# Kernel tuning notes

Hardware: AMD Instinct MI355X
Metric: run time of the kernel (lower is better)

Reference implementation:

```python
import jax, jax.numpy as jnp
import numpy as np

D_MODEL = 768
D_STATE = 128
D_CONV = 4
EXPAND = 2
HEADDIM = 64
NGROUPS = 1
D_INNER = EXPAND * D_MODEL            # 1536
NHEADS = D_INNER // HEADDIM           # 24
CONV_DIM = D_INNER + 2 * NGROUPS * D_STATE  # 1792
D_IN_PROJ = 2 * D_INNER + 2 * NGROUPS * D_STATE + NHEADS  # 3352
EPS = 1e-5


def setup_inputs() -> dict:
    key = jax.random.key(0)
    ks = jax.random.split(key, 8)
    b, l = 4, 2048
    return {
        "feature": jax.random.normal(ks[0], (b, l, D_MODEL), jnp.float32),
        "in_proj_w": jax.random.normal(ks[1], (D_IN_PROJ, D_MODEL), jnp.float32) * 0.02,
        "conv_w": jax.random.normal(ks[2], (CONV_DIM, D_CONV), jnp.float32) * 0.2,
        "conv_b": jnp.zeros((CONV_DIM,), jnp.float32),
        "dt_bias": jax.random.normal(ks[3], (NHEADS,), jnp.float32) * 0.1,
        # A in [1,16) -> A_log = log(A)
        "A_log": jnp.log(1.0 + 15.0 * jax.random.uniform(ks[4], (NHEADS,), jnp.float32)),
        "D": jnp.ones((NHEADS,), jnp.float32),
        "norm_w": jnp.ones((D_INNER,), jnp.float32),
        "out_proj_w": jax.random.normal(ks[5], (D_MODEL, D_INNER), jnp.float32) * 0.02,
        "gate1": jnp.float32(0.6),
    }


def _mamba2(u, in_proj_w, conv_w, conv_b, dt_bias, A_log, D, norm_w, out_proj_w):
    b, l, _ = u.shape
    zxbcdt = jnp.einsum('bld,ed->ble', u, in_proj_w)  # [b,l,3352]
    z, xBC, dt = jnp.split(zxbcdt, [D_INNER, D_INNER + CONV_DIM], axis=-1)
    dt = jax.nn.softplus(dt + dt_bias)  # [b,l,h]

    # causal depthwise conv1d + silu on xBC
    xc = jnp.transpose(xBC, (0, 2, 1))  # [b,c,l]
    xc = jax.lax.conv_general_dilated(
        xc, conv_w[:, None, :], (1,), [(D_CONV - 1, 0)],
        dimension_numbers=('NCH', 'OIH', 'NCH'), feature_group_count=CONV_DIM)
    xBC = jax.nn.silu(jnp.transpose(xc, (0, 2, 1)) + conv_b)

    x, B, C = jnp.split(xBC, [D_INNER, D_INNER + NGROUPS * D_STATE], axis=-1)
    x = x.reshape(b, l, NHEADS, HEADDIM)
    A = -jnp.exp(A_log)          # [h], negative
    dA = jnp.exp(dt * A)         # [b,l,h]

    def step(h, inp):
        # h: [b,h,p,n]
        dA_t, dt_t, x_t, B_t, C_t = inp  # [b,h],[b,h],[b,h,p],[b,n],[b,n]
        h = h * dA_t[..., None, None] + (dt_t[..., None] * x_t)[..., None] * B_t[:, None, None, :]
        y = jnp.einsum('bhpn,bn->bhp', h, C_t)
        return h, y

    h0 = jnp.zeros((b, NHEADS, HEADDIM, D_STATE), u.dtype)
    xs = (jnp.moveaxis(dA, 1, 0), jnp.moveaxis(dt, 1, 0), jnp.moveaxis(x, 1, 0),
          jnp.moveaxis(B, 1, 0), jnp.moveaxis(C, 1, 0))
    _, ys = jax.lax.scan(step, h0, xs)           # [l,b,h,p]
    y = jnp.moveaxis(ys, 0, 1) + x * D[None, None, :, None]
    y = y.reshape(b, l, D_INNER)

    # gated RMSNorm: gate then normalize (norm_before_gate=False)
    y = y * jax.nn.silu(z)
    y = y * jax.lax.rsqrt(jnp.mean(y * y, axis=-1, keepdims=True) + EPS) * norm_w
    return jnp.einsum('bld,ed->ble', y, out_proj_w)


def reference(feature, in_proj_w, conv_w, conv_b, dt_bias, A_log, D, norm_w, out_proj_w, gate1):
    out = _mamba2(feature, in_proj_w, conv_w, conv_b, dt_bias, A_log, D, norm_w, out_proj_w)
    return jax.nn.sigmoid(gate1) * out
```

## Files before the change

kernel.cpp:

```cpp
#include <hip/hip_runtime.h>
#include <cstddef>

#define NB 4
#define SEQL 2048
#define DMODEL 768
#define DSTATE 128
#define HEADDIM 64
#define NHEADS 24
#define DINNER 1536
#define CONVDIM 1792
#define DINPROJ 3352
#define BLROWS (NB*SEQL)
#define RMS_EPS 1e-5f
#define Q 128
#define NC (SEQL/Q)
#define BOFF DINNER
#define COFF (DINNER + DSTATE)
#define BK 64

typedef unsigned int uint;
typedef unsigned short ushort;
typedef __attribute__((ext_vector_type(8))) short bf16x8;
typedef __attribute__((ext_vector_type(4))) float f32x4;

__device__ __forceinline__ float sigmoidf_(float x){ return 1.f/(1.f+expf(-x)); }
__device__ __forceinline__ float siluf_(float x){ return x * sigmoidf_(x); }
__device__ __forceinline__ float softplusf_(float x){ return x > 20.f ? x : log1pf(expf(x)); }

__device__ __forceinline__ ushort f2bf(float f){
    union { float f; uint u; } v; v.f = f;
    uint r = (v.u + 0x7FFFu + ((v.u >> 16) & 1u)) >> 16;
    return (ushort)r;
}
__device__ __forceinline__ float bf2f(ushort s){
    union { uint u; float f; } v; v.u = ((uint)s) << 16;
    return v.f;
}
__device__ __forceinline__ uint pack2(float a, float b){
    return (uint)f2bf(a) | ((uint)f2bf(b) << 16);
}
__device__ __forceinline__ void unpack8(uint4 r, float* o){
    o[0]=bf2f((ushort)(r.x&0xffff)); o[1]=bf2f((ushort)(r.x>>16));
    o[2]=bf2f((ushort)(r.y&0xffff)); o[3]=bf2f((ushort)(r.y>>16));
    o[4]=bf2f((ushort)(r.z&0xffff)); o[5]=bf2f((ushort)(r.z>>16));
    o[6]=bf2f((ushort)(r.w&0xffff)); o[7]=bf2f((ushort)(r.w>>16));
}
__device__ __forceinline__ uint packu2(ushort a, ushort b){
    return (uint)a | ((uint)b << 16);
}

#define GLD16(g, l) __builtin_amdgcn_global_load_lds( \
    (const __attribute__((address_space(1))) void*)(g), \
    (__attribute__((address_space(3))) void*)(l), 16, 0, 0)

__global__ __launch_bounds__(256) void cast_kernel(
    const float* __restrict__ in, ushort* __restrict__ out, int n4)
{
    const int i = blockIdx.x*256 + threadIdx.x;
    if (i < n4) {
        float4 v = ((const float4*)in)[i];
        ushort4 o = make_ushort4(f2bf(v.x), f2bf(v.y), f2bf(v.z), f2bf(v.w));
        ((ushort4*)out)[i] = o;
    }
}

__global__ __launch_bounds__(256) void gemm_mfma(
    const ushort* __restrict__ A, const ushort* __restrict__ W,
    float* __restrict__ C, int M, int N, int K, int nxblk,
    const float* __restrict__ gptr)
{
    __shared__ __align__(16) ushort sm[2*128*BK*2];
    const int tid = threadIdx.x;
    const int wv = tid >> 6, ln = tid & 63;
    const int id = blockIdx.x;
    const int xcd = id & 7;
    const int local = id >> 3;
    const int m0 = (xcd*8 + (local & 7)) * 128;
    const int n0 = (local >> 3) * 128;
    const int wm = (wv >> 1) * 64, wn = (wv & 1) * 64;

    const int sr = ln >> 3;
    const int scol = ((ln & 7) ^ sr) * 8;
    const ushort* gA[4]; const ushort* gB[4];
    ushort* lA[4]; ushort* lB[4];
#pragma unroll
    for (int iss = 0; iss < 4; ++iss) {
        const int ra = m0 + wv*32 + iss*8 + sr;
        gA[iss] = A + (size_t)ra * K + scol;
        int rb = n0 + wv*32 + iss*8 + sr; if (rb >= N) rb = N - 1;
        gB[iss] = W + (size_t)rb * K + scol;
        lA[iss] = &sm[(wv*32 + iss*8) * BK];
        lB[iss] = &sm[8192 + (wv*32 + iss*8) * BK];
    }

    f32x4 acc[4][4];
#pragma unroll
    for (int i = 0; i < 4; ++i)
#pragma unroll
        for (int j = 0; j < 4; ++j) acc[i][j] = (f32x4){0.f, 0.f, 0.f, 0.f};

    const int fr = ln & 15;
    const int fq = ln >> 4;
    const int nt = K / BK;

#pragma unroll
    for (int iss = 0; iss < 4; ++iss) {
        GLD16(gA[iss], lA[iss]);
        GLD16(gB[iss], lB[iss]);
    }

    for (int kt = 0; kt < nt; ++kt) {
        if (kt + 1 < nt) {
            const int so = ((kt + 1) & 1) * 16384;
            const int ko = (kt + 1) * BK;
#pragma unroll
            for (int iss = 0; iss < 4; ++iss) {
                GLD16(gA[iss] + ko, lA[iss] + so);
                GLD16(gB[iss] + ko, lB[iss] + so);
            }
            asm volatile("s_waitcnt vmcnt(8)" ::: "memory");
        } else {
            asm volatile("s_waitcnt vmcnt(0)" ::: "memory");
        }
        __builtin_amdgcn_s_barrier();
        const ushort* As = sm + (kt & 1) * 16384;
        const ushort* Bs = As + 8192;
#pragma unroll
        for (int kh = 0; kh < 2; ++kh) {
            const int sw = ((kh*4 + fq) ^ (fr & 7)) * 8;
            bf16x8 af[4], bfr[4];
#pragma unroll
            for (int i = 0; i < 4; ++i)
                af[i] = *(const bf16x8*)&As[(wm + i*16 + fr)*BK + sw];
#pragma unroll
            for (int j = 0; j < 4; ++j)
                bfr[j] = *(const bf16x8*)&Bs[(wn + j*16 + fr)*BK + sw];
#pragma unroll
            for (int i = 0; i < 4; ++i)
#pragma unroll
                for (int j = 0; j < 4; ++j)
                    acc[i][j] = __builtin_amdgcn_mfma_f32_16x16x32_bf16(af[i], bfr[j], acc[i][j], 0, 0, 0);
        }
        __builtin_amdgcn_s_barrier();
    }

    float scale = 1.f;
    if (gptr) scale = sigmoidf_(*gptr);
    const int cn = ln & 15;
    const int cr = (ln >> 4) * 4;
#pragma unroll
    for (int i = 0; i < 4; ++i) {
        const int mb = m0 + wm + i*16 + cr;
#pragma unroll
        for (int j = 0; j < 4; ++j) {
            const int n = n0 + wn + j*16 + cn;
            if (n < N) {
                float* cp = C + (size_t)mb * N + n;
                cp[0*(size_t)N] = acc[i][j].x * scale;
                cp[1*(size_t)N] = acc[i][j].y * scale;
                cp[2*(size_t)N] = acc[i][j].z * scale;
                cp[3*(size_t)N] = acc[i][j].w * scale;
            }
        }
    }
}

__global__ __launch_bounds__(256) void gemm_mfma_bf16o(
    const ushort* __restrict__ A, const ushort* __restrict__ W,
    ushort* __restrict__ C, float* __restrict__ dtraw, int M, int N, int K)
{
    __shared__ __align__(16) ushort sm[2*128*BK*2];
    const int tid = threadIdx.x;
    const int wv = tid >> 6, ln = tid & 63;
    const int id = blockIdx.x;
    const int xcd = id & 7;
    const int local = id >> 3;
    const int m0 = (xcd*8 + (local & 7)) * 128;
    const int n0 = (local >> 3) * 128;
    const int wm = (wv >> 1) * 64, wn = (wv & 1) * 64;

    const int sr = ln >> 3;
    const int scol = ((ln & 7) ^ sr) * 8;
    const ushort* gA[4]; const ushort* gB[4];
    ushort* lA[4]; ushort* lB[4];
#pragma unroll
    for (int iss = 0; iss < 4; ++iss) {
        const int ra = m0 + wv*32 + iss*8 + sr;
        gA[iss] = A + (size_t)ra * K + scol;
        int rb = n0 + wv*32 + iss*8 + sr; if (rb >= N) rb = N - 1;
        gB[iss] = W + (size_t)rb * K + scol;
        lA[iss] = &sm[(wv*32 + iss*8) * BK];
        lB[iss] = &sm[8192 + (wv*32 + iss*8) * BK];
    }

    f32x4 acc[4][4];
#pragma unroll
    for (int i = 0; i < 4; ++i)
#pragma unroll
        for (int j = 0; j < 4; ++j) acc[i][j] = (f32x4){0.f, 0.f, 0.f, 0.f};

    const int fr = ln & 15;
    const int fq = ln >> 4;
    const int nt = K / BK;

#pragma unroll
    for (int iss = 0; iss < 4; ++iss) {
        GLD16(gA[iss], lA[iss]);
        GLD16(gB[iss], lB[iss]);
    }

    for (int kt = 0; kt < nt; ++kt) {
        if (kt + 1 < nt) {
            const int so = ((kt + 1) & 1) * 16384;
            const int ko = (kt + 1) * BK;
#pragma unroll
            for (int iss = 0; iss < 4; ++iss) {
                GLD16(gA[iss] + ko, lA[iss] + so);
                GLD16(gB[iss] + ko, lB[iss] + so);
            }
            asm volatile("s_waitcnt vmcnt(8)" ::: "memory");
        } else {
            asm volatile("s_waitcnt vmcnt(0)" ::: "memory");
        }
        __builtin_amdgcn_s_barrier();
        const ushort* As = sm + (kt & 1) * 16384;
        const ushort* Bs = As + 8192;
#pragma unroll
        for (int kh = 0; kh < 2; ++kh) {
            const int sw = ((kh*4 + fq) ^ (fr & 7)) * 8;
            bf16x8 af[4], bfr[4];
#pragma unroll
            for (int i = 0; i < 4; ++i)
                af[i] = *(const bf16x8*)&As[(wm + i*16 + fr)*BK + sw];
#pragma unroll
            for (int j = 0; j < 4; ++j)
                bfr[j] = *(const bf16x8*)&Bs[(wn + j*16 + fr)*BK + sw];
#pragma unroll
            for (int i = 0; i < 4; ++i)
#pragma unroll
                for (int j = 0; j < 4; ++j)
                    acc[i][j] = __builtin_amdgcn_mfma_f32_16x16x32_bf16(af[i], bfr[j], acc[i][j], 0, 0, 0);
        }
        __builtin_amdgcn_s_barrier();
    }

    const int cn = ln & 15;
    const int cr = (ln >> 4) * 4;
    __syncthreads();
    ushort* rp = sm + wv*4096;
#pragma unroll
    for (int i = 0; i < 4; ++i)
#pragma unroll
        for (int j = 0; j < 4; ++j) {
            const int col = j*16 + cn;
#pragma unroll
            for (int r = 0; r < 4; ++r)
                rp[(i*16 + cr + r)*64 + col] = f2bf(acc[i][j][r]);
        }
    __syncthreads();
#pragma unroll
    for (int k2 = 0; k2 < 8; ++k2) {
        const int row = k2*8 + (ln >> 3);
        uint4 v = *(const uint4*)&rp[row*64 + (ln & 7)*8];
        const int gm = m0 + wm + row;
        const int gn = n0 + wn + (ln & 7)*8;
        if (gn + 8 <= N)
            *(uint4*)(C + (size_t)gm*N + gn) = v;
    }
    if (n0 + 128 > N) {
#pragma unroll
        for (int i = 0; i < 4; ++i) {
            const int mb = m0 + wm + i*16 + cr;
#pragma unroll
            for (int j = 0; j < 4; ++j) {
                const int col = (n0 + wn + j*16 + cn) - (N - 24);
                if (col >= 0 && col < 24) {
                    dtraw[(size_t)(mb+0)*24 + col] = acc[i][j].x;
                    dtraw[(size_t)(mb+1)*24 + col] = acc[i][j].y;
                    dtraw[(size_t)(mb+2)*24 + col] = acc[i][j].z;
                    dtraw[(size_t)(mb+3)*24 + col] = acc[i][j].w;
                }
            }
        }
    }
}

__global__ __launch_bounds__(448) void conv_kernel(
    const ushort* __restrict__ zx, const float* __restrict__ conv_w,
    const float* __restrict__ conv_b, ushort* __restrict__ xconv)
{
    const int c4 = threadIdx.x;
    const int bl = blockIdx.x;
    const int l = bl & (SEQL - 1);
    float w[4][4];
#pragma unroll
    for (int j = 0; j < 4; ++j) {
        float4 wr = *(const float4*)(conv_w + (c4*4 + j)*4);
        w[j][0]=wr.x; w[j][1]=wr.y; w[j][2]=wr.z; w[j][3]=wr.w;
    }
    float4 bias = *(const float4*)(conv_b + c4*4);
    float s[4] = {bias.x, bias.y, bias.z, bias.w};
#pragma unroll
    for (int k = 0; k < 4; ++k) {
        const int ls = l - 3 + k;
        if (ls >= 0) {
            ushort4 xv = *(const ushort4*)(zx + (size_t)(bl - 3 + k)*DINPROJ + DINNER + c4*4);
            s[0] = fmaf(bf2f(xv.x), w[0][k], s[0]);
            s[1] = fmaf(bf2f(xv.y), w[1][k], s[1]);
            s[2] = fmaf(bf2f(xv.z), w[2][k], s[2]);
            s[3] = fmaf(bf2f(xv.w), w[3][k], s[3]);
        }
    }
    ushort4 o = make_ushort4(f2bf(siluf_(s[0])), f2bf(siluf_(s[1])),
                             f2bf(siluf_(s[2])), f2bf(siluf_(s[3])));
    *(ushort4*)(xconv + (size_t)bl*CONVDIM + c4*4) = o;
}

__global__ __launch_bounds__(128) void dtscan_kernel(
    const float* __restrict__ dtraw, const float* __restrict__ dt_bias,
    const float* __restrict__ A_log, float* __restrict__ dtc, float* __restrict__ clog)
{
    const int c = blockIdx.x, h = blockIdx.y, b = blockIdx.z;
    const int t = threadIdx.x;
    const int bl = b*SEQL + c*Q + t;
    float draw = dtraw[(size_t)bl*24 + h] + dt_bias[h];
    float dtv = softplusf_(draw);
    float la = -expf(A_log[h]) * dtv;
    const int lane = t & 63;
    float v = la;
#pragma unroll
    for (int off = 1; off < 64; off <<= 1) {
        float u = __shfl_up(v, off);
        if (lane >= off) v += u;
    }
    __shared__ float w0tot;
    if (t == 63) w0tot = v;
    __syncthreads();
    if (t >= 64) v += w0tot;
    const int idx = (b*NHEADS + h)*SEQL + c*Q + t;
    dtc[idx] = dtv;
    clog[idx] = v;
}

__global__ __launch_bounds__(256) void gcb_mfma(
    const ushort* __restrict__ xconv, ushort* __restrict__ G)
{
    __shared__ __align__(16) ushort Ca[64*32];
    __shared__ __align__(16) ushort Bb[128*32];
    const int thalf = blockIdx.x, c = blockIdx.y, b = blockIdx.z;
    const int tid = threadIdx.x;
    const int wv = tid >> 6, ln = tid & 63;
    const int fr = ln & 15, fq = ln >> 4, fk = fq*8;
    const int bl0 = b*SEQL + c*Q;
    const int th0 = thalf*64;

    const int sat = tid & 63,  sac = (tid >> 6)*8;
    const int sbt = tid & 127, sbh = (tid >> 7)*16;

    f32x4 acc[4][2];
#pragma unroll
    for (int i = 0; i < 4; ++i)
#pragma unroll
        for (int j = 0; j < 2; ++j) acc[i][j] = (f32x4){0.f,0.f,0.f,0.f};

    for (int ks = 0; ks < 4; ++ks) {
        uint4 av = *(const uint4*)(xconv + (size_t)(bl0 + th0 + sat)*CONVDIM + COFF + ks*32 + sac);
        const ushort* br = xconv + (size_t)(bl0 + sbt)*CONVDIM + BOFF + ks*32 + sbh;
        uint4 bv0 = *(const uint4*)br;
        uint4 bv1 = *(const uint4*)(br + 8);
        __syncthreads();
        *(uint4*)&Ca[sat*32 + sac] = av;
        *(uint4*)&Bb[sbt*32 + sbh] = bv0;
        *(uint4*)&Bb[sbt*32 + sbh + 8] = bv1;
        __syncthreads();
        bf16x8 av_[4], bv_[2];
#pragma unroll
        for (int i = 0; i < 4; ++i)
            av_[i] = *(const bf16x8*)&Ca[(i*16 + fr)*32 + fk];
#pragma unroll
        for (int j = 0; j < 2; ++j)
            bv_[j] = *(const bf16x8*)&Bb[(wv*32 + j*16 + fr)*32 + fk];
#pragma unroll
        for (int i = 0; i < 4; ++i)
#pragma unroll
            for (int j = 0; j < 2; ++j)
                acc[i][j] = __builtin_amdgcn_mfma_f32_16x16x32_bf16(av_[i], bv_[j], acc[i][j], 0, 0, 0);
    }
    ushort* gout = G + (size_t)(b*NC + c)*(Q*Q);
#pragma unroll
    for (int i = 0; i < 4; ++i) {
#pragma unroll
        for (int j = 0; j < 2; ++j) {
            const int s = wv*32 + j*16 + fr;
#pragma unroll
            for (int r = 0; r < 4; ++r) {
                const int t = th0 + i*16 + fq*4 + r;
                gout[t*Q + s] = f2bf(acc[i][j][r]);
            }
        }
    }
}

#define ASTR 40
#define BSTR 40
__global__ __launch_bounds__(256) void locstate_mfma(
    const ushort* __restrict__ xconv, const float* __restrict__ dtc,
    const float* __restrict__ clog, ushort* __restrict__ Sloc)
{
    __shared__ __align__(16) ushort Ab[64*ASTR];
    __shared__ __align__(16) ushort Bb[128*BSTR];
    __shared__ float sw[Q];
    const int c = blockIdx.x, h = blockIdx.y, b = blockIdx.z;
    const int tid = threadIdx.x;
    const int wv = tid >> 6, ln = tid & 63;
    const int fr = ln & 15, fq = ln >> 4, fk = fq*8;
    const int bh = b*NHEADS + h;
    const int bl0 = b*SEQL + c*Q;

    if (tid < Q) {
        const float ce = clog[(size_t)bh*SEQL + c*Q + (Q-1)];
        const float cs = clog[(size_t)bh*SEQL + c*Q + tid];
        sw[tid] = dtc[(size_t)bh*SEQL + c*Q + tid] * expf(ce - cs);
    }
    __syncthreads();

    f32x4 acc[4][2];
#pragma unroll
    for (int i = 0; i < 4; ++i)
#pragma unroll
        for (int j = 0; j < 2; ++j) acc[i][j] = (f32x4){0.f,0.f,0.f,0.f};

    const int ap = tid & 63, aoct = tid >> 6;
    const int bn = tid & 127, bhalf = tid >> 7;

    for (int ks = 0; ks < 4; ++ks) {
        float xv[8];
#pragma unroll
        for (int j = 0; j < 8; ++j) {
            const int s = ks*32 + aoct*8 + j;
            xv[j] = bf2f(xconv[(size_t)(bl0 + s)*CONVDIM + h*HEADDIM + ap]) * sw[s];
        }
        ushort bu[16];
#pragma unroll
        for (int j = 0; j < 16; ++j) {
            const int s = ks*32 + bhalf*16 + j;
            bu[j] = xconv[(size_t)(bl0 + s)*CONVDIM + BOFF + bn];
        }
        __syncthreads();
        *(uint4*)&Ab[ap*ASTR + aoct*8] =
            make_uint4(pack2(xv[0],xv[1]), pack2(xv[2],xv[3]),
                       pack2(xv[4],xv[5]), pack2(xv[6],xv[7]));
        *(uint4*)&Bb[bn*BSTR + bhalf*16] =
            make_uint4(packu2(bu[0],bu[1]), packu2(bu[2],bu[3]),
                       packu2(bu[4],bu[5]), packu2(bu[6],bu[7]));
        *(uint4*)&Bb[bn*BSTR + bhalf*16 + 8] =
            make_uint4(packu2(bu[8],bu[9]), packu2(bu[10],bu[11]),
                       packu2(bu[12],bu[13]), packu2(bu[14],bu[15]));
        __syncthreads();
        bf16x8 af[4], bf[2];
#pragma unroll
        for (int i = 0; i < 4; ++i)
            af[i] = *(const bf16x8*)&Ab[(i*16 + fr)*ASTR + fk];
#pragma unroll
        for (int j = 0; j < 2; ++j)
            bf[j] = *(const bf16x8*)&Bb[(wv*32 + j*16 + fr)*BSTR + fk];
#pragma unroll
        for (int i = 0; i < 4; ++i)
#pragma unroll
            for (int j = 0; j < 2; ++j)
                acc[i][j] = __builtin_amdgcn_mfma_f32_16x16x32_bf16(af[i], bf[j], acc[i][j], 0, 0, 0);
    }
    ushort* dst = Sloc + (size_t)((b*NC + c)*NHEADS + h) * (HEADDIM*DSTATE);
#pragma unroll
    for (int i = 0; i < 4; ++i) {
#pragma unroll
        for (int j = 0; j < 2; ++j) {
            const int n = wv*32 + j*16 + fr;
#pragma unroll
            for (int r = 0; r < 4; ++r) {
                const int p = i*16 + fq*4 + r;
                dst[p*DSTATE + n] = f2bf(acc[i][j][r]);
            }
        }
    }
}

__global__ __launch_bounds__(256) void chunkscan_kernel(
    const float* __restrict__ clog, ushort* __restrict__ S)
{
    const int h = blockIdx.x, b = blockIdx.y, pg = blockIdx.z;
    const int tid = threadIdx.x;
    const int p = pg*16 + (tid >> 4);
    const int n0 = (tid & 15) * 8;
    const int bh = b*NHEADS + h;
    float st[8];
#pragma unroll
    for (int j = 0; j < 8; ++j) st[j] = 0.f;

    for (int c = 0; c < NC; ++c) {
        const float tc = expf(clog[(size_t)bh*SEQL + c*Q + (Q-1)]);
        ushort* base = S + (size_t)((b*NC + c)*NHEADS + h) * (HEADDIM*DSTATE);
        uint4 raw = *(uint4*)(base + p*DSTATE + n0);
        float lv[8];
        unpack8(raw, lv);
        uint4 pre = make_uint4(pack2(st[0],st[1]), pack2(st[2],st[3]),
                               pack2(st[4],st[5]), pack2(st[6],st[7]));
        *(uint4*)(base + p*DSTATE + n0) = pre;
#pragma unroll
        for (int j = 0; j < 8; ++j) st[j] = fmaf(tc, st[j], lv[j]);
    }
}

__global__ __launch_bounds__(256) void ychunk_mfma(
    const ushort* __restrict__ xconv, const float* __restrict__ dtc,
    const float* __restrict__ clog, const ushort* __restrict__ G,
    const ushort* __restrict__ Sp, const float* __restrict__ Dv,
    ushort* __restrict__ ybf)
{
    __shared__ __align__(16) ushort smu[8192];
    ushort* Ab = smu;
    ushort* Bb = smu + 4096;
    __shared__ float s_clog[Q];
    __shared__ float s_dtc[Q];
    const int c = blockIdx.x, h = blockIdx.y, b = blockIdx.z;
    const int tid = threadIdx.x;
    const int wv = tid >> 6, ln = tid & 63;
    const int bh = b*NHEADS + h;
    const int bl0 = b*SEQL + c*Q;
    const int fr = ln & 15, fq = ln >> 4, fk = fq*8;

    if (tid < Q) {
        s_clog[tid] = clog[(size_t)bh*SEQL + c*Q + tid];
        s_dtc[tid]  = dtc [(size_t)bh*SEQL + c*Q + tid];
    }

    f32x4 acc[2][4];
#pragma unroll
    for (int i = 0; i < 2; ++i)
#pragma unroll
        for (int j = 0; j < 4; ++j) acc[i][j] = (f32x4){0.f,0.f,0.f,0.f};

    const int sgt = tid & 127, sgh = (tid >> 7)*16;
    const int sbp = tid & 63,  sbc = (tid >> 6)*8;
    const ushort* spb = Sp + (size_t)((b*NC + c)*NHEADS + h)*(HEADDIM*DSTATE);

    for (int ks = 0; ks < 4; ++ks) {
        const ushort* cr = xconv + (size_t)(bl0 + sgt)*CONVDIM + COFF + ks*32 + sgh;
        uint4 cv0 = *(const uint4*)cr;
        uint4 cv1 = *(const uint4*)(cr + 8);
        uint4 sv = *(const uint4*)(spb + sbp*DSTATE + ks*32 + sbc);
        __syncthreads();
        *(uint4*)&Ab[sgt*32 + sgh]     = cv0;
        *(uint4*)&Ab[sgt*32 + sgh + 8] = cv1;
        *(uint4*)&Bb[sbp*32 + sbc] = sv;
        __syncthreads();
        bf16x8 af[2], bv[4];
        af[0] = *(const bf16x8*)&Ab[(wv*32 +      fr)*32 + fk];
        af[1] = *(const bf16x8*)&Ab[(wv*32 + 16 + fr)*32 + fk];
#pragma unroll
        for (int j = 0; j < 4; ++j)
            bv[j] = *(const bf16x8*)&Bb[(j*16 + fr)*32 + fk];
#pragma unroll
        for (int i = 0; i < 2; ++i)
#pragma unroll
            for (int j = 0; j < 4; ++j)
                acc[i][j] = __builtin_amdgcn_mfma_f32_16x16x32_bf16(af[i], bv[j], acc[i][j], 0, 0, 0);
    }
#pragma unroll
    for (int i = 0; i < 2; ++i) {
        const int tb = wv*32 + i*16 + fq*4;
        float e0 = expf(s_clog[tb+0]), e1 = expf(s_clog[tb+1]);
        float e2 = expf(s_clog[tb+2]), e3 = expf(s_clog[tb+3]);
#pragma unroll
        for (int j = 0; j < 4; ++j) {
            acc[i][j].x *= e0; acc[i][j].y *= e1; acc[i][j].z *= e2; acc[i][j].w *= e3;
        }
    }

    const ushort* gp = G + (size_t)(b*NC + c)*(Q*Q);
    for (int ks = 0; ks < 4; ++ks) {
        uint4 g0 = *(const uint4*)(gp + sgt*Q + ks*32 + sgh);
        uint4 g1 = *(const uint4*)(gp + sgt*Q + ks*32 + sgh + 8);
        ushort xu[8];
#pragma unroll
        for (int j = 0; j < 8; ++j)
            xu[j] = xconv[(size_t)(bl0 + ks*32 + sbc + j)*CONVDIM + h*HEADDIM + sbp];
        __syncthreads();
        {
            float gvals[16];
            unpack8(g0, gvals);
            unpack8(g1, gvals + 8);
            const float ct = s_clog[sgt];
            ushort gw[16];
#pragma unroll
            for (int j = 0; j < 16; ++j) {
                const int s = ks*32 + sgh + j;
                float w = 0.f;
                if (s <= sgt) w = s_dtc[s] * expf(ct - s_clog[s]);
                gw[j] = f2bf(gvals[j] * w);
            }
            *(uint4*)&Ab[sgt*32 + sgh] =
                make_uint4(packu2(gw[0],gw[1]), packu2(gw[2],gw[3]),
                           packu2(gw[4],gw[5]), packu2(gw[6],gw[7]));
            *(uint4*)&Ab[sgt*32 + sgh + 8] =
                make_uint4(packu2(gw[8],gw[9]), packu2(gw[10],gw[11]),
                           packu2(gw[12],gw[13]), packu2(gw[14],gw[15]));
            *(uint4*)&Bb[sbp*32 + sbc] =
                make_uint4(packu2(xu[0],xu[1]), packu2(xu[2],xu[3]),
                           packu2(xu[4],xu[5]), packu2(xu[6],xu[7]));
        }
        __syncthreads();
        if (ks <= wv) {
            bf16x8 af[2], bv[4];
            af[0] = *(const bf16x8*)&Ab[(wv*32 +      fr)*32 + fk];
            af[1] = *(const bf16x8*)&Ab[(wv*32 + 16 + fr)*32 + fk];
#pragma unroll
            for (int j = 0; j < 4; ++j)
                bv[j] = *(const bf16x8*)&Bb[(j*16 + fr)*32 + fk];
#pragma unroll
            for (int i = 0; i < 2; ++i)
#pragma unroll
                for (int j = 0; j < 4; ++j)
                    acc[i][j] = __builtin_amdgcn_mfma_f32_16x16x32_bf16(af[i], bv[j], acc[i][j], 0, 0, 0);
        }
    }

    const float Dh = Dv[h];
    __syncthreads();
    ushort* rp = smu;
#pragma unroll
    for (int i = 0; i < 2; ++i) {
#pragma unroll
        for (int r = 0; r < 4; ++r) {
            const int t = wv*32 + i*16 + fq*4 + r;
            const ushort* xr = xconv + (size_t)(bl0 + t)*CONVDIM + h*HEADDIM;
#pragma unroll
            for (int j = 0; j < 4; ++j) {
                const int p = j*16 + fr;
                rp[t*64 + p] = f2bf(acc[i][j][r] + Dh * bf2f(xr[p]));
            }
        }
    }
#pragma unroll
    for (int k2 = 0; k2 < 4; ++k2) {
        const int row = wv*32 + k2*8 + (ln >> 3);
        uint4 v = *(const uint4*)&rp[row*64 + (ln & 7)*8];
        *(uint4*)(ybf + (size_t)(bl0 + row)*DINNER + h*HEADDIM + (ln & 7)*8) = v;
    }
}

__global__ __launch_bounds__(128) void rms_kernel(
    const ushort* __restrict__ zx, const float* __restrict__ norm_w,
    ushort* __restrict__ ybf)
{
    const int row = blockIdx.x;
    const int tid = threadIdx.x;
    const ushort* zr = zx + (size_t)row * DINPROJ;
    ushort* yr = ybf + (size_t)row * DINNER;
    float v[12];
    float ss = 0.f;
#pragma unroll
    for (int i = 0; i < 3; ++i) {
        const int o = (tid + i*128) * 4;
        ushort4 yv = *(const ushort4*)(yr + o);
        ushort4 zv = *(const ushort4*)(zr + o);
        float a = bf2f(yv.x) * siluf_(bf2f(zv.x));
        float b = bf2f(yv.y) * siluf_(bf2f(zv.y));
        float cc = bf2f(yv.z) * siluf_(bf2f(zv.z));
        float d = bf2f(yv.w) * siluf_(bf2f(zv.w));
        v[i*4+0]=a; v[i*4+1]=b; v[i*4+2]=cc; v[i*4+3]=d;
        ss += a*a + b*b + cc*cc + d*d;
    }
#pragma unroll
    for (int off = 1; off < 64; off <<= 1) ss += __shfl_xor(ss, off);
    __shared__ float red[2];
    if ((tid & 63) == 0) red[tid >> 6] = ss;
    __syncthreads();
    const float rstd = rsqrtf((red[0] + red[1]) * (1.f/DINNER) + RMS_EPS);
#pragma unroll
    for (int i = 0; i < 3; ++i) {
        const int o = (tid + i*128) * 4;
        float4 wv = *(const float4*)(norm_w + o);
        ushort4 ov = make_ushort4(f2bf(v[i*4+0]*rstd*wv.x), f2bf(v[i*4+1]*rstd*wv.y),
                                  f2bf(v[i*4+2]*rstd*wv.z), f2bf(v[i*4+3]*rstd*wv.w));
        *(ushort4*)(yr + o) = ov;
    }
}

extern "C" void kernel_launch(void* const* d_in, const int* in_sizes, int n_in,
                              void* d_out, int out_size, void* d_ws, size_t ws_size,
                              hipStream_t stream)
{
    const float* feature    = (const float*)d_in[0];
    const float* in_proj_w  = (const float*)d_in[1];
    const float* conv_w     = (const float*)d_in[2];
    const float* conv_b     = (const float*)d_in[3];
    const float* dt_bias    = (const float*)d_in[4];
    const float* A_log      = (const float*)d_in[5];
    const float* Dvec       = (const float*)d_in[6];
    const float* norm_w     = (const float*)d_in[7];
    const float* out_proj_w = (const float*)d_in[8];
    const float* gate1      = (const float*)d_in[9];
    float* out = (float*)d_out;

    ushort* zx    = (ushort*)d_ws;
    ushort* xconv = zx + (size_t)BLROWS * DINPROJ;
    ushort* ybf   = xconv + (size_t)BLROWS * CONVDIM;
    float* dtraw  = (float*)(ybf + (size_t)BLROWS * DINNER);
    float* dtc    = dtraw + (size_t)BLROWS * 24;
    float* clog   = dtc + (size_t)NB * NHEADS * SEQL;
    ushort* Gbuf  = (ushort*)(clog + (size_t)NB * NHEADS * SEQL);
    ushort* Sbuf  = Gbuf + (size_t)NB * NC * Q * Q;
    ushort* Abf    = Gbuf;
    ushort* Wbf_in = Gbuf + (size_t)BLROWS * DMODEL;
    ushort* Wbf_out = zx;

    cast_kernel<<<dim3((BLROWS*DMODEL/4 + 255)/256), 256, 0, stream>>>(feature, Abf, BLROWS*DMODEL/4);
    cast_kernel<<<dim3((DINPROJ*DMODEL/4 + 255)/256), 256, 0, stream>>>(in_proj_w, Wbf_in, DINPROJ*DMODEL/4);
    gemm_mfma_bf16o<<<dim3(27*64), 256, 0, stream>>>(Abf, Wbf_in, zx, dtraw,
                                                     BLROWS, DINPROJ, DMODEL);
    conv_kernel<<<dim3(BLROWS), 448, 0, stream>>>(zx, conv_w, conv_b, xconv);
    dtscan_kernel<<<dim3(NC, NHEADS, NB), 128, 0, stream>>>(dtraw, dt_bias, A_log, dtc, clog);
    gcb_mfma<<<dim3(2, NC, NB), 256, 0, stream>>>(xconv, Gbuf);
    locstate_mfma<<<dim3(NC, NHEADS, NB), 256, 0, stream>>>(xconv, dtc, clog, Sbuf);
    chunkscan_kernel<<<dim3(NHEADS, NB, 4), 256, 0, stream>>>(clog, Sbuf);
    ychunk_mfma<<<dim3(NC, NHEADS, NB), 256, 0, stream>>>(xconv, dtc, clog, Gbuf, Sbuf, Dvec, ybf);
    rms_kernel<<<dim3(BLROWS), 128, 0, stream>>>(zx, norm_w, ybf);
    cast_kernel<<<dim3((DMODEL*DINNER/4 + 255)/256), 256, 0, stream>>>(out_proj_w, Wbf_out, DMODEL*DINNER/4);
    gemm_mfma<<<dim3(6*64), 256, 0, stream>>>(ybf, Wbf_out, out,
                                              BLROWS, DMODEL, DINNER, 6, gate1);
}
```

Baseline: 308.4 us.

## Narrow out-proj GEMM tiles, swizzle epilogue LDS, and sliding-window conv over 16 rows

The output projection GEMM now uses 128x64 tiles, giving 768 blocks instead of 384 so more of the compute units are busy on the N=768 problem. The bf16-output GEMM epilogue XOR-swizzles its LDS staging buffer to avoid bank conflicts on the transposed readback. The conv kernel now has each block process 16 consecutive rows and keep a register sliding window, which cuts the redundant reads of the 3 previous rows. The trade-off is lower per-block data reuse in the out GEMM and fewer conv blocks, each with a longer serial loop.

After: 285.8 us. 1.08x faster.

```diff
diff --git a/kernel.cpp b/kernel.cpp
--- a/kernel.cpp
+++ b/kernel.cpp
@@ -66,8 +66,107 @@
 
 __global__ __launch_bounds__(256) void gemm_mfma(
     const ushort* __restrict__ A, const ushort* __restrict__ W,
-    float* __restrict__ C, int M, int N, int K, int nxblk,
+    float* __restrict__ C, int M, int N, int K,
     const float* __restrict__ gptr)
+{
+    __shared__ __align__(16) ushort sm[2*12288];
+    const int tid = threadIdx.x;
+    const int wv = tid >> 6, ln = tid & 63;
+    const int id = blockIdx.x;
+    const int xcd = id & 7;
+    const int local = id >> 3;
+    const int m0 = (xcd*8 + (local & 7)) * 128;
+    const int n0 = (local >> 3) * 64;
+    const int wm = (wv >> 1) * 64, wn = (wv & 1) * 32;
+
+    const int sr = ln >> 3;
+    const int scol = ((ln & 7) ^ sr) * 8;
+    const ushort* gA[4]; ushort* lA[4];
+#pragma unroll
+    for (int iss = 0; iss < 4; ++iss) {
+        gA[iss] = A + (size_t)(m0 + wv*32 + iss*8 + sr) * K + scol;
+        lA[iss] = &sm[(wv*32 + iss*8) * BK];
+    }
+    const ushort* gB[2]; ushort* lB[2];
+#pragma unroll
+    for (int iss = 0; iss < 2; ++iss) {
+        gB[iss] = W + (size_t)(n0 + wv*16 + iss*8 + sr) * K + scol;
+        lB[iss] = &sm[8192 + (wv*16 + iss*8) * BK];
+    }
+
+    f32x4 acc[4][2];
+#pragma unroll
+    for (int i = 0; i < 4; ++i)
+#pragma unroll
+        for (int j = 0; j < 2; ++j) acc[i][j] = (f32x4){0.f, 0.f, 0.f, 0.f};
+
+    const int fr = ln & 15;
+    const int fq = ln >> 4;
+    const int nt = K / BK;
+
+#pragma unroll
+    for (int iss = 0; iss < 4; ++iss) GLD16(gA[iss], lA[iss]);
+#pragma unroll
+    for (int iss = 0; iss < 2; ++iss) GLD16(gB[iss], lB[iss]);
+
+    for (int kt = 0; kt < nt; ++kt) {
+        if (kt + 1 < nt) {
+            const int so = ((kt + 1) & 1) * 12288;
+            const int ko = (kt + 1) * BK;
+#pragma unroll
+            for (int iss = 0; iss < 4; ++iss) GLD16(gA[iss] + ko, lA[iss] + so);
+#pragma unroll
+            for (int iss = 0; iss < 2; ++iss) GLD16(gB[iss] + ko, lB[iss] + so);
+            asm volatile("s_waitcnt vmcnt(6)" ::: "memory");
+        } else {
+            asm volatile("s_waitcnt vmcnt(0)" ::: "memory");
+        }
+        __builtin_amdgcn_s_barrier();
+        const ushort* As = sm + (kt & 1) * 12288;
+        const ushort* Bs = As + 8192;
+#pragma unroll
+        for (int kh = 0; kh < 2; ++kh) {
+            const int sw = ((kh*4 + fq) ^ (fr & 7)) * 8;
+            bf16x8 af[4], bfr[2];
+#pragma unroll
+            for (int i = 0; i < 4; ++i)
+                af[i] = *(const bf16x8*)&As[(wm + i*16 + fr)*BK + sw];
+#pragma unroll
+            for (int j = 0; j < 2; ++j)
+                bfr[j] = *(const bf16x8*)&Bs[(wn + j*16 + fr)*BK + sw];
+#pragma unroll
+            for (int i = 0; i < 4; ++i)
+#pragma unroll
+                for (int j = 0; j < 2; ++j)
+                    acc[i][j] = __builtin_amdgcn_mfma_f32_16x16x32_bf16(af[i], bfr[j], acc[i][j], 0, 0, 0);
+        }
+        __builtin_amdgcn_s_barrier();
+    }
+
+    float scale = 1.f;
+    if (gptr) scale = sigmoidf_(*gptr);
+    const int cn = ln & 15;
+    const int cr = (ln >> 4) * 4;
+#pragma unroll
+    for (int i = 0; i < 4; ++i) {
+        const int mb = m0 + wm + i*16 + cr;
+#pragma unroll
+        for (int j = 0; j < 2; ++j) {
+            const int n = n0 + wn + j*16 + cn;
+            if (n < N) {
+                float* cp = C + (size_t)mb * N + n;
+                cp[0*(size_t)N] = acc[i][j].x * scale;
+                cp[1*(size_t)N] = acc[i][j].y * scale;
+                cp[2*(size_t)N] = acc[i][j].z * scale;
+                cp[3*(size_t)N] = acc[i][j].w * scale;
+            }
+        }
+    }
+}
+
+__global__ __launch_bounds__(256) void gemm_mfma_bf16o(
+    const ushort* __restrict__ A, const ushort* __restrict__ W,
+    ushort* __restrict__ C, float* __restrict__ dtraw, int M, int N, int K)
 {
     __shared__ __align__(16) ushort sm[2*128*BK*2];
     const int tid = threadIdx.x;
@@ -144,106 +243,6 @@
         __builtin_amdgcn_s_barrier();
     }
 
-    float scale = 1.f;
-    if (gptr) scale = sigmoidf_(*gptr);
-    const int cn = ln & 15;
-    const int cr = (ln >> 4) * 4;
-#pragma unroll
-    for (int i = 0; i < 4; ++i) {
-        const int mb = m0 + wm + i*16 + cr;
-#pragma unroll
-        for (int j = 0; j < 4; ++j) {
-            const int n = n0 + wn + j*16 + cn;
-            if (n < N) {
-                float* cp = C + (size_t)mb * N + n;
-                cp[0*(size_t)N] = acc[i][j].x * scale;
-                cp[1*(size_t)N] = acc[i][j].y * scale;
-                cp[2*(size_t)N] = acc[i][j].z * scale;
-                cp[3*(size_t)N] = acc[i][j].w * scale;
-            }
-        }
-    }
-}
-
-__global__ __launch_bounds__(256) void gemm_mfma_bf16o(
-    const ushort* __restrict__ A, const ushort* __restrict__ W,
-    ushort* __restrict__ C, float* __restrict__ dtraw, int M, int N, int K)
-{
-    __shared__ __align__(16) ushort sm[2*128*BK*2];
-    const int tid = threadIdx.x;
-    const int wv = tid >> 6, ln = tid & 63;
-    const int id = blockIdx.x;
-    const int xcd = id & 7;
-    const int local = id >> 3;
-    const int m0 = (xcd*8 + (local & 7)) * 128;
-    const int n0 = (local >> 3) * 128;
-    const int wm = (wv >> 1) * 64, wn = (wv & 1) * 64;
-
-    const int sr = ln >> 3;
-    const int scol = ((ln & 7) ^ sr) * 8;
-    const ushort* gA[4]; const ushort* gB[4];
-    ushort* lA[4]; ushort* lB[4];
-#pragma unroll
-    for (int iss = 0; iss < 4; ++iss) {
-        const int ra = m0 + wv*32 + iss*8 + sr;
-        gA[iss] = A + (size_t)ra * K + scol;
-        int rb = n0 + wv*32 + iss*8 + sr; if (rb >= N) rb = N - 1;
-        gB[iss] = W + (size_t)rb * K + scol;
-        lA[iss] = &sm[(wv*32 + iss*8) * BK];
-        lB[iss] = &sm[8192 + (wv*32 + iss*8) * BK];
-    }
-
-    f32x4 acc[4][4];
-#pragma unroll
-    for (int i = 0; i < 4; ++i)
-#pragma unroll
-        for (int j = 0; j < 4; ++j) acc[i][j] = (f32x4){0.f, 0.f, 0.f, 0.f};
-
-    const int fr = ln & 15;
-    const int fq = ln >> 4;
-    const int nt = K / BK;
-
-#pragma unroll
-    for (int iss = 0; iss < 4; ++iss) {
-        GLD16(gA[iss], lA[iss]);
-        GLD16(gB[iss], lB[iss]);
-    }
-
-    for (int kt = 0; kt < nt; ++kt) {
-        if (kt + 1 < nt) {
-            const int so = ((kt + 1) & 1) * 16384;
-            const int ko = (kt + 1) * BK;
-#pragma unroll
-            for (int iss = 0; iss < 4; ++iss) {
-                GLD16(gA[iss] + ko, lA[iss] + so);
-                GLD16(gB[iss] + ko, lB[iss] + so);
-            }
-            asm volatile("s_waitcnt vmcnt(8)" ::: "memory");
-        } else {
-            asm volatile("s_waitcnt vmcnt(0)" ::: "memory");
-        }
-        __builtin_amdgcn_s_barrier();
-        const ushort* As = sm + (kt & 1) * 16384;
-        const ushort* Bs = As + 8192;
-#pragma unroll
-        for (int kh = 0; kh < 2; ++kh) {
-            const int sw = ((kh*4 + fq) ^ (fr & 7)) * 8;
-            bf16x8 af[4], bfr[4];
-#pragma unroll
-            for (int i = 0; i < 4; ++i)
-                af[i] = *(const bf16x8*)&As[(wm + i*16 + fr)*BK + sw];
-#pragma unroll
-            for (int j = 0; j < 4; ++j)
-                bfr[j] = *(const bf16x8*)&Bs[(wn + j*16 + fr)*BK + sw];
-#pragma unroll
-            for (int i = 0; i < 4; ++i)
-#pragma unroll
-                for (int j = 0; j < 4; ++j)
-                    acc[i][j] = __builtin_amdgcn_mfma_f32_16x16x32_bf16(af[i], bfr[j], acc[i][j], 0, 0, 0);
-        }
-        __builtin_amdgcn_s_barrier();
-    }
-
     const int cn = ln & 15;
     const int cr = (ln >> 4) * 4;
     __syncthreads();
@@ -252,18 +251,21 @@
     for (int i = 0; i < 4; ++i)
 #pragma unroll
         for (int j = 0; j < 4; ++j) {
-            const int col = j*16 + cn;
-#pragma unroll
-            for (int r = 0; r < 4; ++r)
-                rp[(i*16 + cr + r)*64 + col] = f2bf(acc[i][j][r]);
+            const int colb = j*16 + cn;
+#pragma unroll
+            for (int r = 0; r < 4; ++r) {
+                const int row = i*16 + cr + r;
+                rp[row*64 + (((colb >> 3) ^ (row & 7)) * 8) + (colb & 7)] = f2bf(acc[i][j][r]);
+            }
         }
     __syncthreads();
 #pragma unroll
     for (int k2 = 0; k2 < 8; ++k2) {
         const int row = k2*8 + (ln >> 3);
-        uint4 v = *(const uint4*)&rp[row*64 + (ln & 7)*8];
+        const int cg = ln & 7;
+        uint4 v = *(const uint4*)&rp[row*64 + ((cg ^ (row & 7)) * 8)];
         const int gm = m0 + wm + row;
-        const int gn = n0 + wn + (ln & 7)*8;
+        const int gn = n0 + wn + cg*8;
         if (gn + 8 <= N)
             *(uint4*)(C + (size_t)gm*N + gn) = v;
     }
@@ -290,30 +292,44 @@
     const float* __restrict__ conv_b, ushort* __restrict__ xconv)
 {
     const int c4 = threadIdx.x;
-    const int bl = blockIdx.x;
-    const int l = bl & (SEQL - 1);
+    const int bl0 = blockIdx.x * 16;
+    const int l0 = bl0 & (SEQL - 1);
     float w[4][4];
 #pragma unroll
     for (int j = 0; j < 4; ++j) {
         float4 wr = *(const float4*)(conv_w + (c4*4 + j)*4);
         w[j][0]=wr.x; w[j][1]=wr.y; w[j][2]=wr.z; w[j][3]=wr.w;
     }
-    float4 bias = *(const float4*)(conv_b + c4*4);
-    float s[4] = {bias.x, bias.y, bias.z, bias.w};
-#pragma unroll
-    for (int k = 0; k < 4; ++k) {
-        const int ls = l - 3 + k;
-        if (ls >= 0) {
-            ushort4 xv = *(const ushort4*)(zx + (size_t)(bl - 3 + k)*DINPROJ + DINNER + c4*4);
-            s[0] = fmaf(bf2f(xv.x), w[0][k], s[0]);
-            s[1] = fmaf(bf2f(xv.y), w[1][k], s[1]);
-            s[2] = fmaf(bf2f(xv.z), w[2][k], s[2]);
-            s[3] = fmaf(bf2f(xv.w), w[3][k], s[3]);
-        }
-    }
-    ushort4 o = make_ushort4(f2bf(siluf_(s[0])), f2bf(siluf_(s[1])),
-                             f2bf(siluf_(s[2])), f2bf(siluf_(s[3])));
-    *(ushort4*)(xconv + (size_t)bl*CONVDIM + c4*4) = o;
+    const float4 bias = *(const float4*)(conv_b + c4*4);
+    const ushort* src = zx + DINNER + (size_t)c4*4;
+    ushort* dst = xconv + (size_t)c4*4;
+
+    float h0[4], h1[4], h2[4];
+    if (l0 == 0) {
+#pragma unroll
+        for (int ch = 0; ch < 4; ++ch) { h0[ch]=0.f; h1[ch]=0.f; h2[ch]=0.f; }
+    } else {
+        ushort4 a = *(const ushort4*)(src + (size_t)(bl0-3)*DINPROJ);
+        ushort4 b = *(const ushort4*)(src + (size_t)(bl0-2)*DINPROJ);
+        ushort4 c = *(const ushort4*)(src + (size_t)(bl0-1)*DINPROJ);
+        h0[0]=bf2f(a.x); h0[1]=bf2f(a.y); h0[2]=bf2f(a.z); h0[3]=bf2f(a.w);
+        h1[0]=bf2f(b.x); h1[1]=bf2f(b.y); h1[2]=bf2f(b.z); h1[3]=bf2f(b.w);
+        h2[0]=bf2f(c.x); h2[1]=bf2f(c.y); h2[2]=bf2f(c.z); h2[3]=bf2f(c.w);
+    }
+#pragma unroll
+    for (int t = 0; t < 16; ++t) {
+        ushort4 xv = *(const ushort4*)(src + (size_t)(bl0 + t)*DINPROJ);
+        float h3[4] = {bf2f(xv.x), bf2f(xv.y), bf2f(xv.z), bf2f(xv.w)};
+        float s0 = fmaf(h3[0], w[0][3], fmaf(h2[0], w[0][2], fmaf(h1[0], w[0][1], fmaf(h0[0], w[0][0], bias.x))));
+        float s1 = fmaf(h3[1], w[1][3], fmaf(h2[1], w[1][2], fmaf(h1[1], w[1][1], fmaf(h0[1], w[1][0], bias.y))));
+        float s2 = fmaf(h3[2], w[2][3], fmaf(h2[2], w[2][2], fmaf(h1[2], w[2][1], fmaf(h0[2], w[2][0], bias.z))));
+        float s3 = fmaf(h3[3], w[3][3], fmaf(h2[3], w[3][2], fmaf(h1[3], w[3][1], fmaf(h0[3], w[3][0], bias.w))));
+        ushort4 o = make_ushort4(f2bf(siluf_(s0)), f2bf(siluf_(s1)),
+                                 f2bf(siluf_(s2)), f2bf(siluf_(s3)));
+        *(ushort4*)(dst + (size_t)(bl0 + t)*CONVDIM) = o;
+#pragma unroll
+        for (int ch = 0; ch < 4; ++ch) { h0[ch]=h1[ch]; h1[ch]=h2[ch]; h2[ch]=h3[ch]; }
+    }
 }
 
 __global__ __launch_bounds__(128) void dtscan_kernel(
@@ -719,7 +735,7 @@
     cast_kernel<<<dim3((DINPROJ*DMODEL/4 + 255)/256), 256, 0, stream>>>(in_proj_w, Wbf_in, DINPROJ*DMODEL/4);
     gemm_mfma_bf16o<<<dim3(27*64), 256, 0, stream>>>(Abf, Wbf_in, zx, dtraw,
                                                      BLROWS, DINPROJ, DMODEL);
-    conv_kernel<<<dim3(BLROWS), 448, 0, stream>>>(zx, conv_w, conv_b, xconv);
+    conv_kernel<<<dim3(BLROWS/16), 448, 0, stream>>>(zx, conv_w, conv_b, xconv);
     dtscan_kernel<<<dim3(NC, NHEADS, NB), 128, 0, stream>>>(dtraw, dt_bias, A_log, dtc, clog);
     gcb_mfma<<<dim3(2, NC, NB), 256, 0, stream>>>(xconv, Gbuf);
     locstate_mfma<<<dim3(NC, NHEADS, NB), 256, 0, stream>>>(xconv, dtc, clog, Sbuf);
@@ -727,6 +743,6 @@
     ychunk_mfma<<<dim3(NC, NHEADS, NB), 256, 0, stream>>>(xconv, dtc, clog, Gbuf, Sbuf, Dvec, ybf);
     rms_kernel<<<dim3(BLROWS), 128, 0, stream>>>(zx, norm_w, ybf);
     cast_kernel<<<dim3((DMODEL*DINNER/4 + 255)/256), 256, 0, stream>>>(out_proj_w, Wbf_out, DMODEL*DINNER/4);
-    gemm_mfma<<<dim3(6*64), 256, 0, stream>>>(ybf, Wbf_out, out,
-                                              BLROWS, DMODEL, DINNER, 6, gate1);
-}
+    gemm_mfma<<<dim3(768), 256, 0, stream>>>(ybf, Wbf_out, out,
+                                             BLROWS, DMODEL, DINNER, gate1);
+}
```
